# Performance work log

Hardware: AMD Instinct MI355X
Metric: run time of the kernel (lower is better)

The kernel has to match this reference:

```python
import jax, jax.numpy as jnp
import numpy as np

H = W = 1536
DT = 0.02
FAST_DT, SLOW_DT = 1.0, 0.2
EPS_FAST, EPS_SLOW = 0.06, 0.02
F2S, S2F = 0.04, 0.02


def setup_inputs() -> dict:
    key = jax.random.key(0)
    k1, k2, k3 = jax.random.split(key, 3)
    phi = jax.random.normal(k1, (1, 10, H, W), jnp.float32)
    sensory_map = jax.random.normal(k2, (1, 1, H, W), jnp.float32)
    gamma = jnp.array([0.2, 0.15, 0.1, 0.18, 0.12, 0.13, 0.14, 0.16, 0.11, 0.1], jnp.float32)
    alpha = jnp.array([0.3, 0.25, 0.22, 0.18, 0.2, 0.15, 0.19, 0.24, 0.17, 0.16], jnp.float32)
    mix_w = jax.random.normal(k3, (10, 10), jnp.float32) * 0.1  # 1x1 conv weight, no bias
    return {"phi": phi, "sensory_map": sensory_map, "gamma": gamma, "alpha": alpha, "mix_w": mix_w}


def _lap(x):
    # periodic 5-point Laplacian via rolls on the last two (spatial) dims
    return (jnp.roll(x, 1, -2) + jnp.roll(x, -1, -2)
            + jnp.roll(x, 1, -1) + jnp.roll(x, -1, -1) - 4.0 * x)


def _step(phi, sensory_map, gamma, alpha, mix_w):
    lap = _lap(phi)
    bilap = _lap(lap)
    g, a, p = gamma, alpha, phi
    ch = [
        -g[0] * lap[:, 0] - a[0] * p[:, 0] ** 3 + 0.12 * bilap[:, 0],
        -g[1] * lap[:, 1] + 0.15 * jnp.sin(p[:, 1]) + 0.08 * p[:, 1] ** 3,
        -g[2] * lap[:, 2] + 0.2 * p[:, 2] * (1.0 - p[:, 2] ** 2),
        -g[3] * lap[:, 3] - 0.03 * p[:, 3] ** 5 + 0.08 * bilap[:, 3],
        -g[4] * lap[:, 4] + 0.12 * p[:, 4] * jnp.log(jnp.abs(p[:, 4]) + 1e-6) + 0.02 * bilap[:, 4],
        -g[5] * lap[:, 5] + 0.08 * p[:, 5] ** 3 - 0.02 * p[:, 5] ** 5,
        -g[6] * lap[:, 6] + 0.06 * p[:, 6] ** 4 - 0.04 * p[:, 6],
        -g[7] * lap[:, 7] + 0.08 * jnp.sinh(jnp.clip(p[:, 7], -2.0, 2.0)),
        -g[8] * lap[:, 8] + 0.05 * p[:, 8] ** 2 - 0.08 * p[:, 8],
        -g[9] * lap[:, 9] + 0.02 * p[:, 9] ** 6 - 0.04 * p[:, 9] ** 3 + 0.01 * bilap[:, 9],
    ]
    dphi = jnp.stack(ch, axis=1)                                 # [1,10,H,W]
    coupling = jnp.einsum('oc,bchw->bohw', mix_w, phi)            # 1x1 conv, no bias
    fast_mean = phi[:, :5].mean(axis=1, keepdims=True)            # [1,1,H,W]
    slow_mean = phi[:, 5:].mean(axis=1, keepdims=True)
    sd = sensory_map[:, 0]                                        # [1,H,W]
    dphi_f = dphi[:, :5] + EPS_FAST * coupling[:, :5] + S2F * slow_mean
    dphi_s = dphi[:, 5:] + EPS_SLOW * coupling[:, 5:] + F2S * fast_mean
    dphi_f = dphi_f.at[:, 0].add(0.2 * sd).at[:, 4].add(0.08 * jnp.abs(sd))
    dphi_s = dphi_s.at[:, 4].add(0.05 * sd)                       # global channel 9
    phi_next = jnp.concatenate([phi[:, :5] + DT * FAST_DT * dphi_f,
                                phi[:, 5:] + DT * SLOW_DT * dphi_s], axis=1)
    return jnp.clip(phi_next, -4.0, 4.0)


def reference(phi, sensory_map, gamma, alpha, mix_w):
    phi_next = _step(phi, sensory_map, gamma, alpha, mix_w)
    phi1_mean = phi_next[:, 0].mean(axis=(1, 2))
    phi5_mean = phi_next[:, 4].mean(axis=(1, 2))
    field_means = phi_next.mean(axis=(2, 3))
    return phi_next, phi1_mean, phi5_mean, field_means
```

## Files before the change

### kernel.cpp

```cpp
#include <hip/hip_runtime.h>
#include <math.h>

#define HH 1536
#define WW 1536
#define HWSZ (HH*WW)

__global__ __launch_bounds__(256) void step_kernel(
    const float* __restrict__ phi,
    const float* __restrict__ sensory,
    const float* __restrict__ gamma,
    const float* __restrict__ alpha,
    const float* __restrict__ mixw,
    float* __restrict__ out,
    float* __restrict__ sums)
{
    __shared__ float s_mix[100];
    __shared__ float s_g[10];
    __shared__ float s_a0;
    const int tid = threadIdx.x;
    if (tid < 100) s_mix[tid] = mixw[tid];
    if (tid < 10)  s_g[tid]   = gamma[tid];
    if (tid == 0)  s_a0       = alpha[0];
    __syncthreads();

    const int x = blockIdx.x * 256 + tid;
    const int y = blockIdx.y;

    const int xm1 = (x == 0)      ? WW - 1     : x - 1;
    const int xp1 = (x == WW - 1) ? 0          : x + 1;
    const int xm2 = (x < 2)       ? x + WW - 2 : x - 2;
    const int xp2 = (x >= WW - 2) ? x - WW + 2 : x + 2;
    const int ym1 = (y == 0)      ? HH - 1     : y - 1;
    const int yp1 = (y == HH - 1) ? 0          : y + 1;
    const int ym2 = (y < 2)       ? y + HH - 2 : y - 2;
    const int yp2 = (y >= HH - 2) ? y - HH + 2 : y + 2;

    const int r0  = y   * WW;
    const int rm1 = ym1 * WW;
    const int rp1 = yp1 * WW;
    const int rm2 = ym2 * WW;
    const int rp2 = yp2 * WW;

    float p[10], lap[10], bl[10];
    #pragma unroll
    for (int c = 0; c < 10; ++c) {
        const float* pc = phi + (size_t)c * HWSZ;
        const float c0 = pc[r0 + x];
        const float nn = pc[rm1 + x];
        const float ss = pc[rp1 + x];
        const float wv = pc[r0 + xm1];
        const float ee = pc[r0 + xp1];
        const float s1 = nn + ss + wv + ee;
        p[c]   = c0;
        lap[c] = s1 - 4.0f * c0;
        if (c == 0 || c == 3 || c == 4 || c == 9) {
            const float d1 = pc[rm1 + xm1];
            const float d2 = pc[rm1 + xp1];
            const float d3 = pc[rp1 + xm1];
            const float d4 = pc[rp1 + xp1];
            const float t1 = pc[rm2 + x];
            const float t2 = pc[rp2 + x];
            const float t3 = pc[r0 + xm2];
            const float t4 = pc[r0 + xp2];
            bl[c] = 20.0f * c0 - 8.0f * s1 + 2.0f * (d1 + d2 + d3 + d4) + (t1 + t2 + t3 + t4);
        } else {
            bl[c] = 0.0f;
        }
    }

    float d[10];
    {
        const float p0 = p[0];
        d[0] = -s_g[0]*lap[0] - s_a0*p0*p0*p0 + 0.12f*bl[0];
        const float p1 = p[1];
        d[1] = -s_g[1]*lap[1] + 0.15f*sinf(p1) + 0.08f*p1*p1*p1;
        const float p2 = p[2];
        d[2] = -s_g[2]*lap[2] + 0.2f*p2*(1.0f - p2*p2);
        const float p3 = p[3];
        const float p3_2 = p3*p3;
        d[3] = -s_g[3]*lap[3] - 0.03f*p3_2*p3_2*p3 + 0.08f*bl[3];
        const float p4 = p[4];
        d[4] = -s_g[4]*lap[4] + 0.12f*p4*logf(fabsf(p4) + 1e-6f) + 0.02f*bl[4];
        const float p5 = p[5];
        const float p5_2 = p5*p5;
        d[5] = -s_g[5]*lap[5] + 0.08f*p5_2*p5 - 0.02f*p5_2*p5_2*p5;
        const float p6 = p[6];
        const float p6_2 = p6*p6;
        d[6] = -s_g[6]*lap[6] + 0.06f*p6_2*p6_2 - 0.04f*p6;
        const float p7 = fminf(fmaxf(p[7], -2.0f), 2.0f);
        d[7] = -s_g[7]*lap[7] + 0.08f*sinhf(p7);
        const float p8 = p[8];
        d[8] = -s_g[8]*lap[8] + 0.05f*p8*p8 - 0.08f*p8;
        const float p9 = p[9];
        const float p9_2 = p9*p9;
        const float p9_3 = p9_2*p9;
        d[9] = -s_g[9]*lap[9] + 0.02f*p9_3*p9_3 - 0.04f*p9_3 + 0.01f*bl[9];
    }

    const float fm = (p[0] + p[1] + p[2] + p[3] + p[4]) * 0.2f;
    const float sm = (p[5] + p[6] + p[7] + p[8] + p[9]) * 0.2f;
    const float sd = sensory[r0 + x];

    float pn[10];
    #pragma unroll
    for (int o = 0; o < 10; ++o) {
        float cp = 0.0f;
        #pragma unroll
        for (int c = 0; c < 10; ++c) cp = fmaf(s_mix[o*10 + c], p[c], cp);
        float dd = d[o];
        if (o < 5) {
            dd += 0.06f * cp + 0.02f * sm;
            if (o == 0) dd += 0.2f  * sd;
            if (o == 4) dd += 0.08f * fabsf(sd);
            pn[o] = p[o] + 0.02f * dd;
        } else {
            dd += 0.02f * cp + 0.04f * fm;
            if (o == 9) dd += 0.05f * sd;
            pn[o] = p[o] + 0.004f * dd;
        }
        pn[o] = fminf(fmaxf(pn[o], -4.0f), 4.0f);
        out[(size_t)o * HWSZ + r0 + x] = pn[o];
    }

    const int lane = tid & 63;
    const int wave = tid >> 6;
    __shared__ float s_red[4][10];
    #pragma unroll
    for (int c = 0; c < 10; ++c) {
        float v = pn[c];
        #pragma unroll
        for (int off = 32; off > 0; off >>= 1) v += __shfl_down(v, off, 64);
        if (lane == 0) s_red[wave][c] = v;
    }
    __syncthreads();
    if (tid < 10) {
        const float v = s_red[0][tid] + s_red[1][tid] + s_red[2][tid] + s_red[3][tid];
        atomicAdd(&sums[tid], v);
    }
}

__global__ void finalize_kernel(const float* __restrict__ sums,
                                float* __restrict__ out)
{
    const int t = threadIdx.x;
    const float inv = 1.0f / (float)HWSZ;
    const size_t base = (size_t)10 * HWSZ;
    if (t == 0) out[base]     = sums[0] * inv;
    if (t == 1) out[base + 1] = sums[4] * inv;
    if (t >= 2 && t < 12) out[base + 2 + (t - 2)] = sums[t - 2] * inv;
}

extern "C" void kernel_launch(void* const* d_in, const int* in_sizes, int n_in,
                              void* d_out, int out_size, void* d_ws, size_t ws_size,
                              hipStream_t stream) {
    const float* phi     = (const float*)d_in[0];
    const float* sensory = (const float*)d_in[1];
    const float* gamma   = (const float*)d_in[2];
    const float* alpha   = (const float*)d_in[3];
    const float* mixw    = (const float*)d_in[4];
    float* out = (float*)d_out;
    float* sums = (float*)d_ws;

    hipMemsetAsync(sums, 0, 10 * sizeof(float), stream);

    dim3 grid(WW / 256, HH);
    step_kernel<<<grid, 256, 0, stream>>>(phi, sensory, gamma, alpha, mixw, out, sums);
    finalize_kernel<<<1, 64, 0, stream>>>(sums, out);
}
```

Measured before the change: 277.0 us.

## Process four pixels per thread with float4 loads, one row per block

Each thread now handles four adjacent pixels using float4 loads and stores. Horizontal neighbours come from registers, with only scalar halo loads at the edges, and each 384-thread block covers a full row. Rows are assigned with a swizzled block-to-row mapping. Partial sums are reduced per output channel over four pixels before the wave shuffle, which cuts reduction work and atomics. Per-thread register pressure grows (40 values for pv plus 40 for dv), which may reduce occupancy.

```diff
diff --git a/kernel.cpp b/kernel.cpp
--- a/kernel.cpp
+++ b/kernel.cpp
@@ -4,8 +4,13 @@
 #define HH 1536
 #define WW 1536
 #define HWSZ (HH*WW)
-
-__global__ __launch_bounds__(256) void step_kernel(
+#define NT 384
+
+__device__ __forceinline__ float4 LD4(const float* __restrict__ p, int row, int t) {
+    return reinterpret_cast<const float4*>(p + row)[t];
+}
+
+__global__ __launch_bounds__(NT) void step_kernel(
     const float* __restrict__ phi,
     const float* __restrict__ sensory,
     const float* __restrict__ gamma,
@@ -17,19 +22,19 @@
     __shared__ float s_mix[100];
     __shared__ float s_g[10];
     __shared__ float s_a0;
+    __shared__ float s_red[6][10];
+
     const int tid = threadIdx.x;
     if (tid < 100) s_mix[tid] = mixw[tid];
     if (tid < 10)  s_g[tid]   = gamma[tid];
     if (tid == 0)  s_a0       = alpha[0];
     __syncthreads();
 
-    const int x = blockIdx.x * 256 + tid;
-    const int y = blockIdx.y;
-
-    const int xm1 = (x == 0)      ? WW - 1     : x - 1;
-    const int xp1 = (x == WW - 1) ? 0          : x + 1;
-    const int xm2 = (x < 2)       ? x + WW - 2 : x - 2;
-    const int xp2 = (x >= WW - 2) ? x - WW + 2 : x + 2;
+    const int blk = blockIdx.x;
+    const int y = (blk & 7) * 192 + (blk >> 3);
+
+    const int x0 = tid * 4;
+
     const int ym1 = (y == 0)      ? HH - 1     : y - 1;
     const int yp1 = (y == HH - 1) ? 0          : y + 1;
     const int ym2 = (y < 2)       ? y + HH - 2 : y - 2;
@@ -41,100 +46,127 @@
     const int rm2 = ym2 * WW;
     const int rp2 = yp2 * WW;
 
-    float p[10], lap[10], bl[10];
+    const int xl1 = (x0 == 0)        ? WW - 1 : x0 - 1;
+    const int xl2 = (x0 == 0)        ? WW - 2 : x0 - 2;
+    const int xr1 = (x0 + 4 == WW)   ? 0      : x0 + 4;
+    const int xr2 = (x0 + 4 == WW)   ? 1      : x0 + 5;
+
+    float pv[10][4];
+    float dv[10][4];
+
     #pragma unroll
     for (int c = 0; c < 10; ++c) {
         const float* pc = phi + (size_t)c * HWSZ;
-        const float c0 = pc[r0 + x];
-        const float nn = pc[rm1 + x];
-        const float ss = pc[rp1 + x];
-        const float wv = pc[r0 + xm1];
-        const float ee = pc[r0 + xp1];
-        const float s1 = nn + ss + wv + ee;
-        p[c]   = c0;
-        lap[c] = s1 - 4.0f * c0;
+        const float4 cm = LD4(pc, r0,  tid);
+        const float4 nn = LD4(pc, rm1, tid);
+        const float4 ss = LD4(pc, rp1, tid);
+        const float wl1 = pc[r0 + xl1];
+        const float wr1 = pc[r0 + xr1];
+
+        float lap[4];
+        lap[0] = nn.x + ss.x + wl1  + cm.y - 4.0f * cm.x;
+        lap[1] = nn.y + ss.y + cm.x + cm.z - 4.0f * cm.y;
+        lap[2] = nn.z + ss.z + cm.y + cm.w - 4.0f * cm.z;
+        lap[3] = nn.w + ss.w + cm.z + wr1  - 4.0f * cm.w;
+
+        float bl[4] = {0.f, 0.f, 0.f, 0.f};
         if (c == 0 || c == 3 || c == 4 || c == 9) {
-            const float d1 = pc[rm1 + xm1];
-            const float d2 = pc[rm1 + xp1];
-            const float d3 = pc[rp1 + xm1];
-            const float d4 = pc[rp1 + xp1];
-            const float t1 = pc[rm2 + x];
-            const float t2 = pc[rp2 + x];
-            const float t3 = pc[r0 + xm2];
-            const float t4 = pc[r0 + xp2];
-            bl[c] = 20.0f * c0 - 8.0f * s1 + 2.0f * (d1 + d2 + d3 + d4) + (t1 + t2 + t3 + t4);
-        } else {
-            bl[c] = 0.0f;
-        }
-    }
-
-    float d[10];
+            const float4 t2n = LD4(pc, rm2, tid);
+            const float4 t2s = LD4(pc, rp2, tid);
+            const float wl2 = pc[r0  + xl2];
+            const float wr2 = pc[r0  + xr2];
+            const float nwl = pc[rm1 + xl1];
+            const float ner = pc[rm1 + xr1];
+            const float swl = pc[rp1 + xl1];
+            const float ser = pc[rp1 + xr1];
+            bl[0] = 20.0f*cm.x - 8.0f*(nn.x + ss.x + wl1  + cm.y)
+                  + 2.0f*(nwl  + nn.y + swl  + ss.y) + (t2n.x + t2s.x + wl2  + cm.z);
+            bl[1] = 20.0f*cm.y - 8.0f*(nn.y + ss.y + cm.x + cm.z)
+                  + 2.0f*(nn.x + nn.z + ss.x + ss.z) + (t2n.y + t2s.y + wl1  + cm.w);
+            bl[2] = 20.0f*cm.z - 8.0f*(nn.z + ss.z + cm.y + cm.w)
+                  + 2.0f*(nn.y + nn.w + ss.y + ss.w) + (t2n.z + t2s.z + cm.x + wr1);
+            bl[3] = 20.0f*cm.w - 8.0f*(nn.w + ss.w + cm.z + wr1)
+                  + 2.0f*(nn.z + ner  + ss.z + ser ) + (t2n.w + t2s.w + cm.y + wr2);
+        }
+
+        pv[c][0] = cm.x; pv[c][1] = cm.y; pv[c][2] = cm.z; pv[c][3] = cm.w;
+
+        #pragma unroll
+        for (int k = 0; k < 4; ++k) {
+            const float pp = pv[c][k];
+            const float lv = lap[k];
+            const float bv = bl[k];
+            float dd;
+            switch (c) {
+            case 0: dd = -s_g[0]*lv - s_a0*pp*pp*pp + 0.12f*bv; break;
+            case 1: dd = -s_g[1]*lv + 0.15f*sinf(pp) + 0.08f*pp*pp*pp; break;
+            case 2: dd = -s_g[2]*lv + 0.2f*pp*(1.0f - pp*pp); break;
+            case 3: { const float p2 = pp*pp;
+                      dd = -s_g[3]*lv - 0.03f*p2*p2*pp + 0.08f*bv; } break;
+            case 4: dd = -s_g[4]*lv + 0.12f*pp*logf(fabsf(pp) + 1e-6f) + 0.02f*bv; break;
+            case 5: { const float p2 = pp*pp;
+                      dd = -s_g[5]*lv + 0.08f*p2*pp - 0.02f*p2*p2*pp; } break;
+            case 6: { const float p2 = pp*pp;
+                      dd = -s_g[6]*lv + 0.06f*p2*p2 - 0.04f*pp; } break;
+            case 7: { const float pc7 = fminf(fmaxf(pp, -2.0f), 2.0f);
+                      dd = -s_g[7]*lv + 0.08f*sinhf(pc7); } break;
+            case 8: dd = -s_g[8]*lv + 0.05f*pp*pp - 0.08f*pp; break;
+            default: { const float p3 = pp*pp*pp;
+                       dd = -s_g[9]*lv + 0.02f*p3*p3 - 0.04f*p3 + 0.01f*bv; } break;
+            }
+            dv[c][k] = dd;
+        }
+    }
+
+    float fmv[4], smv[4], sdk[4];
     {
-        const float p0 = p[0];
-        d[0] = -s_g[0]*lap[0] - s_a0*p0*p0*p0 + 0.12f*bl[0];
-        const float p1 = p[1];
-        d[1] = -s_g[1]*lap[1] + 0.15f*sinf(p1) + 0.08f*p1*p1*p1;
-        const float p2 = p[2];
-        d[2] = -s_g[2]*lap[2] + 0.2f*p2*(1.0f - p2*p2);
-        const float p3 = p[3];
-        const float p3_2 = p3*p3;
-        d[3] = -s_g[3]*lap[3] - 0.03f*p3_2*p3_2*p3 + 0.08f*bl[3];
-        const float p4 = p[4];
-        d[4] = -s_g[4]*lap[4] + 0.12f*p4*logf(fabsf(p4) + 1e-6f) + 0.02f*bl[4];
-        const float p5 = p[5];
-        const float p5_2 = p5*p5;
-        d[5] = -s_g[5]*lap[5] + 0.08f*p5_2*p5 - 0.02f*p5_2*p5_2*p5;
-        const float p6 = p[6];
-        const float p6_2 = p6*p6;
-        d[6] = -s_g[6]*lap[6] + 0.06f*p6_2*p6_2 - 0.04f*p6;
-        const float p7 = fminf(fmaxf(p[7], -2.0f), 2.0f);
-        d[7] = -s_g[7]*lap[7] + 0.08f*sinhf(p7);
-        const float p8 = p[8];
-        d[8] = -s_g[8]*lap[8] + 0.05f*p8*p8 - 0.08f*p8;
-        const float p9 = p[9];
-        const float p9_2 = p9*p9;
-        const float p9_3 = p9_2*p9;
-        d[9] = -s_g[9]*lap[9] + 0.02f*p9_3*p9_3 - 0.04f*p9_3 + 0.01f*bl[9];
-    }
-
-    const float fm = (p[0] + p[1] + p[2] + p[3] + p[4]) * 0.2f;
-    const float sm = (p[5] + p[6] + p[7] + p[8] + p[9]) * 0.2f;
-    const float sd = sensory[r0 + x];
-
-    float pn[10];
+        const float4 sd4 = LD4(sensory, r0, tid);
+        sdk[0] = sd4.x; sdk[1] = sd4.y; sdk[2] = sd4.z; sdk[3] = sd4.w;
+        #pragma unroll
+        for (int k = 0; k < 4; ++k) {
+            fmv[k] = (pv[0][k] + pv[1][k] + pv[2][k] + pv[3][k] + pv[4][k]) * 0.2f;
+            smv[k] = (pv[5][k] + pv[6][k] + pv[7][k] + pv[8][k] + pv[9][k]) * 0.2f;
+        }
+    }
+
+    const int lane = tid & 63;
+    const int wave = tid >> 6;
+
     #pragma unroll
     for (int o = 0; o < 10; ++o) {
-        float cp = 0.0f;
-        #pragma unroll
-        for (int c = 0; c < 10; ++c) cp = fmaf(s_mix[o*10 + c], p[c], cp);
-        float dd = d[o];
-        if (o < 5) {
-            dd += 0.06f * cp + 0.02f * sm;
-            if (o == 0) dd += 0.2f  * sd;
-            if (o == 4) dd += 0.08f * fabsf(sd);
-            pn[o] = p[o] + 0.02f * dd;
-        } else {
-            dd += 0.02f * cp + 0.04f * fm;
-            if (o == 9) dd += 0.05f * sd;
-            pn[o] = p[o] + 0.004f * dd;
-        }
-        pn[o] = fminf(fmaxf(pn[o], -4.0f), 4.0f);
-        out[(size_t)o * HWSZ + r0 + x] = pn[o];
-    }
-
-    const int lane = tid & 63;
-    const int wave = tid >> 6;
-    __shared__ float s_red[4][10];
-    #pragma unroll
-    for (int c = 0; c < 10; ++c) {
-        float v = pn[c];
-        #pragma unroll
-        for (int off = 32; off > 0; off >>= 1) v += __shfl_down(v, off, 64);
-        if (lane == 0) s_red[wave][c] = v;
-    }
+        float pn[4];
+        #pragma unroll
+        for (int k = 0; k < 4; ++k) {
+            float cp = 0.0f;
+            #pragma unroll
+            for (int c = 0; c < 10; ++c) cp = fmaf(s_mix[o*10 + c], pv[c][k], cp);
+            float dd = dv[o][k];
+            if (o < 5) {
+                dd += 0.06f * cp + 0.02f * smv[k];
+                if (o == 0) dd += 0.2f  * sdk[k];
+                if (o == 4) dd += 0.08f * fabsf(sdk[k]);
+                pn[k] = pv[o][k] + 0.02f * dd;
+            } else {
+                dd += 0.02f * cp + 0.04f * fmv[k];
+                if (o == 9) dd += 0.05f * sdk[k];
+                pn[k] = pv[o][k] + 0.004f * dd;
+            }
+            pn[k] = fminf(fmaxf(pn[k], -4.0f), 4.0f);
+        }
+        float4 o4; o4.x = pn[0]; o4.y = pn[1]; o4.z = pn[2]; o4.w = pn[3];
+        reinterpret_cast<float4*>(out + (size_t)o * HWSZ + r0)[tid] = o4;
+
+        float s = pn[0] + pn[1] + pn[2] + pn[3];
+        #pragma unroll
+        for (int off = 32; off > 0; off >>= 1) s += __shfl_down(s, off, 64);
+        if (lane == 0) s_red[wave][o] = s;
+    }
+
     __syncthreads();
     if (tid < 10) {
-        const float v = s_red[0][tid] + s_red[1][tid] + s_red[2][tid] + s_red[3][tid];
+        float v = 0.0f;
+        #pragma unroll
+        for (int w = 0; w < 6; ++w) v += s_red[w][tid];
         atomicAdd(&sums[tid], v);
     }
 }
@@ -163,7 +195,6 @@
 
     hipMemsetAsync(sums, 0, 10 * sizeof(float), stream);
 
-    dim3 grid(WW / 256, HH);
-    step_kernel<<<grid, 256, 0, stream>>>(phi, sensory, gamma, alpha, mixw, out, sums);
+    step_kernel<<<dim3(HH), NT, 0, stream>>>(phi, sensory, gamma, alpha, mixw, out, sums);
     finalize_kernel<<<1, 64, 0, stream>>>(sums, out);
 }
```

Measured after the change: 240.2 us. 1.15x faster.
